# Kernel optimization log

Hardware: AMD Instinct MI355X
Metric: run time of the kernel (lower is better)

Reference implementation:

```python
import jax, jax.numpy as jnp
import numpy as np

N = 50000
E = 800000
DZ = 64
DH = 64


def setup_inputs() -> dict:
    key = jax.random.key(0)
    ks = jax.random.split(key, 10)
    z = jax.random.normal(ks[0], (N, DZ), dtype=jnp.float32)
    edge_src = jax.random.randint(ks[1], (E,), 0, N, dtype=jnp.int32)
    edge_dst = jax.random.randint(ks[2], (E,), 0, N, dtype=jnp.int32)
    # weights: normal(0, 0.1); biases: uniform(-0.1, 0.1) as in the torch init
    W_cur = 0.1 * jax.random.normal(ks[3], (DH, DZ), dtype=jnp.float32)
    b_cur = jax.random.uniform(ks[4], (DH,), minval=-0.1, maxval=0.1, dtype=jnp.float32)
    W_nbr = 0.1 * jax.random.normal(ks[5], (DH, 2 * DZ), dtype=jnp.float32)
    b_nbr = jax.random.uniform(ks[6], (DH,), minval=-0.1, maxval=0.1, dtype=jnp.float32)
    W_out = 0.1 * jax.random.normal(ks[7], (DZ, 2 * DH), dtype=jnp.float32)
    b_out = jax.random.uniform(ks[8], (DZ,), minval=-0.1, maxval=0.1, dtype=jnp.float32)
    return {"z": z, "edge_src": edge_src, "edge_dst": edge_dst,
            "W_cur": W_cur, "b_cur": b_cur, "W_nbr": W_nbr, "b_nbr": b_nbr,
            "W_out": W_out, "b_out": b_out}


def reference(z, edge_src, edge_dst, W_cur, b_cur, W_nbr, b_nbr, W_out, b_out):
    # self branch: Sigmoid(Linear(dim_z -> dim_h))  [N, DH]
    curvv = jax.nn.sigmoid(z @ W_cur.T + b_cur)
    # per-edge: concat(z[center], z[neighbor]) -> Sigmoid(Linear)  [E, DH]
    e = jnp.concatenate([z[edge_dst], z[edge_src]], axis=-1)  # [E, 2*DZ]
    m = jax.nn.sigmoid(e @ W_nbr.T + b_nbr)
    # sum-aggregate messages per center node (isolated nodes -> zeros)
    nbrvv = jax.ops.segment_sum(m, edge_dst, num_segments=N)  # [N, DH]
    # fuse: Tanh(Linear(concat(cur, nbr) -> dim_z))
    h = jnp.concatenate([curvv, nbrvv], axis=-1)  # [N, 2*DH]
    dzdt = jnp.tanh(h @ W_out.T + b_out)
    return dzdt
```

## Files before the change

kernel.cpp:

```cpp
#include <hip/hip_runtime.h>
#include <math.h>

#define NN 50000
#define NE 800000
#define BSH 7
#define NBUCK 391
#define CAP 4096
#define CHUNK 4096
#define NCH ((NE + CHUNK - 1) / CHUNK)
#define K1B 782
#define EPT2 8
#define SENT 50000

typedef float4 f4;
typedef float2 f2;
typedef unsigned short u16;
typedef unsigned int u32;

__device__ __forceinline__ float sigf(float x) {
    return __builtin_amdgcn_rcpf(1.0f + __expf(-x));
}

__device__ __forceinline__ u16 f32_to_bf16_rne(float f) {
    unsigned u = __float_as_uint(f);
    u += 0x7FFFu + ((u >> 16) & 1u);
    return (u16)(u >> 16);
}

#define K1_WFLOATS (3 * 32 * 64 * 2)
__global__ __launch_bounds__(512, 4) void k1_sc(
    const float* __restrict__ z,
    const float* __restrict__ Wc, const float* __restrict__ bc,
    const float* __restrict__ Wn, const float* __restrict__ bn,
    float* __restrict__ P, u16* __restrict__ Qh, float* __restrict__ C,
    const int* __restrict__ esrc, const int* __restrict__ edst,
    int* __restrict__ gcur, u32* __restrict__ ebuf)
{
    const int tid = threadIdx.x;
    if (blockIdx.x < K1B) {
        __shared__ float sh[K1_WFLOATS + 8 * 256];
        f2* w2 = (f2*)sh;
        for (int j = tid; j < 3 * 32 * 64; j += 512) {
            const int m = j >> 11, r = j & 2047;
            const int k2 = r >> 6, h = r & 63;
            const float* s = (m == 0) ? (Wc + h * 64 + 2 * k2)
                                      : (Wn + h * 128 + (m - 1) * 64 + 2 * k2);
            w2[(m * 32 + k2) * 64 + h] = *(const f2*)s;
        }
        __syncthreads();

        const int lane = tid & 63;
        const int wid  = tid >> 6;
        f4* tile = (f4*)(sh + K1_WFLOATS) + wid * 64;
        const f2* wl0 = w2;
        const f2* wl1 = w2 + 32 * 64;
        const f2* wl2 = w2 + 2 * 32 * 64;
        const float bcur = bc[lane], bnbr = bn[lane];

        const int gw = blockIdx.x * 8 + wid;
        const int nw = K1B * 8;
        for (int chunk = gw; chunk < NN / 4; chunk += nw) {
            const int n0 = chunk * 4;
            tile[lane] = *(const f4*)(z + n0 * 64 + lane * 4);
            float a0[4], a1[4], a2[4];
            #pragma unroll
            for (int ni = 0; ni < 4; ++ni) { a0[ni] = 0.f; a1[ni] = 0.f; a2[ni] = 0.f; }
            #pragma unroll 2
            for (int k4 = 0; k4 < 16; ++k4) {
                const f2 w0a = wl0[(2 * k4) * 64 + lane], w0b = wl0[(2 * k4 + 1) * 64 + lane];
                const f2 w1a = wl1[(2 * k4) * 64 + lane], w1b = wl1[(2 * k4 + 1) * 64 + lane];
                const f2 w2a = wl2[(2 * k4) * 64 + lane], w2b = wl2[(2 * k4 + 1) * 64 + lane];
                #pragma unroll
                for (int ni = 0; ni < 4; ++ni) {
                    const f4 zz = tile[ni * 16 + k4];
                    a0[ni] = fmaf(w0b.y, zz.w, fmaf(w0b.x, zz.z, fmaf(w0a.y, zz.y, fmaf(w0a.x, zz.x, a0[ni]))));
                    a1[ni] = fmaf(w1b.y, zz.w, fmaf(w1b.x, zz.z, fmaf(w1a.y, zz.y, fmaf(w1a.x, zz.x, a1[ni]))));
                    a2[ni] = fmaf(w2b.y, zz.w, fmaf(w2b.x, zz.z, fmaf(w2a.y, zz.y, fmaf(w2a.x, zz.x, a2[ni]))));
                }
            }
            #pragma unroll
            for (int ni = 0; ni < 4; ++ni) {
                const int n = n0 + ni;
                C[n * 64 + lane]  = sigf(a0[ni] + bcur);
                P[n * 64 + lane]  = a1[ni] + bnbr;
                Qh[n * 64 + lane] = f32_to_bf16_rne(a2[ni]);
            }
        }
    } else {
        if (blockIdx.x == K1B && tid < 64) Qh[(size_t)SENT * 64 + tid] = 0xFF80u;

        __shared__ int cnt[NBUCK];
        __shared__ int gbase[NBUCK];
        __shared__ int lcur[NBUCK];
        for (int i = tid; i < NBUCK; i += 512) cnt[i] = 0;
        __syncthreads();

        const int base = (blockIdx.x - K1B) * CHUNK;
        u32 ent[EPT2];
        int nb[EPT2];
        #pragma unroll
        for (int t = 0; t < EPT2; ++t) {
            const int e = base + t * 512 + tid;
            if (e < NE) {
                const int d = edst[e], s = esrc[e];
                const int b = d >> BSH;
                ent[t] = ((u32)(d & 127) << 16) | (u32)s;
                nb[t] = b;
                atomicAdd(&cnt[b], 1);
            } else {
                nb[t] = -1;
            }
        }
        __syncthreads();
        for (int i = tid; i < NBUCK; i += 512) {
            gbase[i] = cnt[i] ? atomicAdd(&gcur[i], cnt[i]) : 0;
            lcur[i] = 0;
        }
        __syncthreads();
        #pragma unroll
        for (int t = 0; t < EPT2; ++t) {
            if (nb[t] >= 0) {
                const int li = atomicAdd(&lcur[nb[t]], 1);
                ebuf[nb[t] * CAP + gbase[nb[t]] + li] = ent[t];
            }
        }
    }
}

__global__ __launch_bounds__(256) void k_bsort(const int* __restrict__ gcur,
                                               const u32* __restrict__ ebuf,
                                               u32* __restrict__ bd,
                                               u16* __restrict__ ss)
{
    __shared__ int hist[128];
    __shared__ int lcur[128];
    __shared__ int ps[128];
    __shared__ int tot;
    const int b = blockIdx.x;
    const int ecnt = gcur[b];
    const int e0 = b * CAP;
    const int n0 = b << BSH;
    const int t = threadIdx.x;

    if (t < 128) hist[t] = 0;
    __syncthreads();
    for (int j = t; j < ecnt; j += 256)
        atomicAdd(&hist[(ebuf[e0 + j] >> 16) & 127], 1);
    __syncthreads();
    if (t < 128) ps[t] = (hist[t] + 7) & ~7;
    __syncthreads();
    for (int o = 1; o < 128; o <<= 1) {
        int v = 0;
        if (t < 128 && t >= o) v = ps[t - o];
        __syncthreads();
        if (t < 128 && t >= o) ps[t] += v;
        __syncthreads();
    }
    if (t < 128) {
        const int a = hist[t];
        const int r = (a + 7) & ~7;
        const int excl = ps[t] - r;
        lcur[t] = excl;
        const int n = n0 + t;
        if (n < NN) bd[n] = ((u32)(e0 + excl) << 8) | (u32)a;
        if (t == 127) tot = ps[127];
    }
    __syncthreads();
    const int zw = (tot + 48) >> 1;
    u32* ssw = (u32*)(ss + e0);
    for (int j = t; j < zw; j += 256) ssw[j] = 0xC350C350u;
    __syncthreads();
    for (int j = t; j < ecnt; j += 256) {
        const u32 ent = ebuf[e0 + j];
        const int p = atomicAdd(&lcur[(ent >> 16) & 127], 1);
        ss[e0 + p] = (u16)(ent & 0xFFFFu);
    }
}

template<int NQ>
__device__ __forceinline__ void round_g(const u16* __restrict__ ip,
                                        const u16* __restrict__ qbl,
                                        float p, float& acc)
{
    uint4 iv0, iv1, iv2;
    asm volatile("global_load_dwordx4 %0, %1, off" : "=v"(iv0) : "v"(ip));
    if constexpr (NQ >= 16)
        asm volatile("global_load_dwordx4 %0, %1, off offset:16" : "=v"(iv1) : "v"(ip));
    if constexpr (NQ >= 24)
        asm volatile("global_load_dwordx4 %0, %1, off offset:32" : "=v"(iv2) : "v"(ip));
    asm volatile("s_waitcnt vmcnt(0)" ::: "memory");
    __builtin_amdgcn_sched_barrier(0);
    u32 wv[NQ / 2];
    wv[0] = iv0.x; wv[1] = iv0.y; wv[2] = iv0.z; wv[3] = iv0.w;
    if constexpr (NQ >= 16) { wv[4] = iv1.x; wv[5] = iv1.y; wv[6] = iv1.z; wv[7] = iv1.w; }
    if constexpr (NQ >= 24) { wv[8] = iv2.x; wv[9] = iv2.y; wv[10] = iv2.z; wv[11] = iv2.w; }
    u32 q[NQ];
    #pragma unroll
    for (int t8 = 0; t8 < NQ / 2; ++t8) {
        const u16* aL = qbl + ((wv[t8] & 0xFFFFu) << 6);
        const u16* aH = qbl + ((wv[t8] >> 16) << 6);
        asm volatile("global_load_ushort %0, %1, off" : "=v"(q[2 * t8])     : "v"(aL));
        asm volatile("global_load_ushort %0, %1, off" : "=v"(q[2 * t8 + 1]) : "v"(aH));
    }
    asm volatile("s_waitcnt vmcnt(0)" ::: "memory");
    __builtin_amdgcn_sched_barrier(0);
    #pragma unroll
    for (int t = 0; t < NQ; ++t)
        acc += sigf(p + __uint_as_float(q[t] << 16));
}

__global__ __launch_bounds__(512, 8) void k23(
    const u32* __restrict__ bd, const u16* __restrict__ ss,
    const float* __restrict__ P, const u16* __restrict__ Qh,
    const float* __restrict__ C, const float* __restrict__ Wo,
    const float* __restrict__ bo, float* __restrict__ out)
{
    __shared__ u32 w1u[32 * 64];
    __shared__ f2  w2f[32 * 64];
    __shared__ float tiles[8 * 512];
    const int tid = threadIdx.x;
    for (int j = tid; j < 32 * 64; j += 512) {
        const int k2 = j >> 6, d = j & 63;
        const f2 wc = *(const f2*)(Wo + d * 128 + 2 * k2);
        w1u[k2 * 64 + d] = ((u32)f32_to_bf16_rne(wc.y) << 16) | (u32)f32_to_bf16_rne(wc.x);
        w2f[k2 * 64 + d] = *(const f2*)(Wo + d * 128 + 64 + 2 * k2);
    }
    __syncthreads();

    const int lane = tid & 63;
    const int wid  = tid >> 6;
    float* tile = tiles + wid * 512;
    const f4* t4 = (const f4*)tile;
    const u16* qbl = Qh + lane;
    const float bout = bo[lane];

    for (int chunk = blockIdx.x * 8 + wid; chunk < NN / 4; chunk += gridDim.x * 8) {
        const int n0 = chunk * 4;
        #pragma unroll
        for (int i = 0; i < 4; ++i) {
            const int n = n0 + i;
            const u32 w = bd[n];
            const int beg = __builtin_amdgcn_readfirstlane((int)(w >> 8));
            const int dg  = __builtin_amdgcn_readfirstlane((int)(w & 255u));
            const int rdg = (dg + 7) & ~7;
            const float p = P[n * 64 + lane];
            tile[i * 128 + lane] = C[n * 64 + lane];
            float acc = 0.f;

            int jb = 0;
            for (; jb + 24 <= rdg; jb += 24)
                round_g<24>(ss + beg + jb, qbl, p, acc);
            const int rem = rdg - jb;
            if (rem == 16)     round_g<16>(ss + beg + jb, qbl, p, acc);
            else if (rem == 8) round_g<8>(ss + beg + jb, qbl, p, acc);

            tile[i * 128 + 64 + lane] = acc;
        }

        float a2[4] = {0.f, 0.f, 0.f, 0.f};
        #pragma unroll 2
        for (int k4 = 0; k4 < 16; ++k4) {
            const u32 ua = w1u[(2 * k4) * 64 + lane];
            const u32 ub = w1u[(2 * k4 + 1) * 64 + lane];
            const float wa0 = __uint_as_float(ua << 16);
            const float wa1 = __uint_as_float(ua & 0xFFFF0000u);
            const float wb0 = __uint_as_float(ub << 16);
            const float wb1 = __uint_as_float(ub & 0xFFFF0000u);
            #pragma unroll
            for (int i = 0; i < 4; ++i) {
                const f4 hv = t4[i * 32 + k4];
                a2[i] = fmaf(wb1, hv.w, fmaf(wb0, hv.z, fmaf(wa1, hv.y, fmaf(wa0, hv.x, a2[i]))));
            }
        }
        #pragma unroll 2
        for (int k4 = 0; k4 < 16; ++k4) {
            const f2 wa = w2f[(2 * k4) * 64 + lane];
            const f2 wb = w2f[(2 * k4 + 1) * 64 + lane];
            #pragma unroll
            for (int i = 0; i < 4; ++i) {
                const f4 hv = t4[i * 32 + 16 + k4];
                a2[i] = fmaf(wb.y, hv.w, fmaf(wb.x, hv.z, fmaf(wa.y, hv.y, fmaf(wa.x, hv.x, a2[i]))));
            }
        }
        #pragma unroll
        for (int i = 0; i < 4; ++i)
            out[(n0 + i) * 64 + lane] = tanhf(a2[i] + bout);
    }
}

extern "C" void kernel_launch(void* const* d_in, const int* in_sizes, int n_in,
                              void* d_out, int out_size, void* d_ws, size_t ws_size,
                              hipStream_t stream) {
    const float* z  = (const float*)d_in[0];
    const int* esrc = (const int*)d_in[1];
    const int* edst = (const int*)d_in[2];
    const float* Wc = (const float*)d_in[3];
    const float* bc = (const float*)d_in[4];
    const float* Wn = (const float*)d_in[5];
    const float* bn = (const float*)d_in[6];
    const float* Wo = (const float*)d_in[7];
    const float* bo = (const float*)d_in[8];
    float* out = (float*)d_out;

    float* P   = (float*)d_ws;
    float* C   = P + (size_t)NN * 64;
    u16* Qh    = (u16*)(C + (size_t)NN * 64);
    u32* bd    = (u32*)(Qh + (size_t)(NN + 1) * 64);
    int* gcur  = (int*)(bd + NN + 64);
    u32* ebuf  = (u32*)(gcur + 512);
    u16* ss    = (u16*)(ebuf + (size_t)NBUCK * CAP);

    hipMemsetAsync(gcur, 0, 512 * sizeof(int), stream);
    k1_sc<<<K1B + NCH, 512, 0, stream>>>(z, Wc, bc, Wn, bn, P, Qh, C,
                                         esrc, edst, gcur, ebuf);
    k_bsort<<<NBUCK, 256, 0, stream>>>(gcur, ebuf, bd, ss);
    k23<<<1563, 512, 0, stream>>>(bd, ss, P, Qh, C, Wo, bo, out);
}
```

Baseline: 106.6 us.

## Prefetch next node's edge indices and prescale logits for raw exp2 sigmoid

Every node's padded edge list now takes at least 24 slots, so the gather kernel can issue one fixed 24-wide round per node and prefetch the next node's index block while the current Q gathers are in flight. Outlier nodes with more than 24 edges fall back to the old loop. P and Q are pre-multiplied by -log2(e) so the sigmoid can use v_exp_f32 directly, dropping a multiply per edge, and the sentinel changes to +inf so padded slots still contribute zero. The cost is more padding, so more sentinel gathers and more wasted sigmoids for low-degree nodes (average degree is about 16), plus a larger padded index buffer.

Result: slower. 109.3 us (+2.6%).

```diff
diff --git a/kernel.cpp b/kernel.cpp
--- a/kernel.cpp
+++ b/kernel.cpp
@@ -11,6 +11,7 @@
 #define K1B 782
 #define EPT2 8
 #define SENT 50000
+#define NL2E -1.4426950408889634f
 
 typedef float4 f4;
 typedef float2 f2;
@@ -19,6 +20,12 @@
 
 __device__ __forceinline__ float sigf(float x) {
     return __builtin_amdgcn_rcpf(1.0f + __expf(-x));
+}
+
+__device__ __forceinline__ float sigf2(float y) {
+    float e;
+    asm("v_exp_f32 %0, %1" : "=v"(e) : "v"(y));
+    return __builtin_amdgcn_rcpf(1.0f + e);
 }
 
 __device__ __forceinline__ u16 f32_to_bf16_rne(float f) {
@@ -82,12 +89,12 @@
             for (int ni = 0; ni < 4; ++ni) {
                 const int n = n0 + ni;
                 C[n * 64 + lane]  = sigf(a0[ni] + bcur);
-                P[n * 64 + lane]  = a1[ni] + bnbr;
-                Qh[n * 64 + lane] = f32_to_bf16_rne(a2[ni]);
+                P[n * 64 + lane]  = (a1[ni] + bnbr) * NL2E;
+                Qh[n * 64 + lane] = f32_to_bf16_rne(a2[ni] * NL2E);
             }
         }
     } else {
-        if (blockIdx.x == K1B && tid < 64) Qh[(size_t)SENT * 64 + tid] = 0xFF80u;
+        if (blockIdx.x == K1B && tid < 64) Qh[(size_t)SENT * 64 + tid] = 0x7F80u;
 
         __shared__ int cnt[NBUCK];
         __shared__ int gbase[NBUCK];
@@ -147,7 +154,10 @@
     for (int j = t; j < ecnt; j += 256)
         atomicAdd(&hist[(ebuf[e0 + j] >> 16) & 127], 1);
     __syncthreads();
-    if (t < 128) ps[t] = (hist[t] + 7) & ~7;
+    if (t < 128) {
+        const int a = hist[t];
+        ps[t] = (a <= 24) ? 24 : ((a + 7) & ~7);
+    }
     __syncthreads();
     for (int o = 1; o < 128; o <<= 1) {
         int v = 0;
@@ -158,7 +168,7 @@
     }
     if (t < 128) {
         const int a = hist[t];
-        const int r = (a + 7) & ~7;
+        const int r = (a <= 24) ? 24 : ((a + 7) & ~7);
         const int excl = ps[t] - r;
         lcur[t] = excl;
         const int n = n0 + t;
@@ -206,7 +216,7 @@
     __builtin_amdgcn_sched_barrier(0);
     #pragma unroll
     for (int t = 0; t < NQ; ++t)
-        acc += sigf(p + __uint_as_float(q[t] << 16));
+        acc += sigf2(p + __uint_as_float(q[t] << 16));
 }
 
 __global__ __launch_bounds__(512, 8) void k23(
@@ -236,24 +246,61 @@
 
     for (int chunk = blockIdx.x * 8 + wid; chunk < NN / 4; chunk += gridDim.x * 8) {
         const int n0 = chunk * 4;
+        int beg[4], dg[4];
+        float pv[4];
         #pragma unroll
         for (int i = 0; i < 4; ++i) {
-            const int n = n0 + i;
-            const u32 w = bd[n];
-            const int beg = __builtin_amdgcn_readfirstlane((int)(w >> 8));
-            const int dg  = __builtin_amdgcn_readfirstlane((int)(w & 255u));
-            const int rdg = (dg + 7) & ~7;
-            const float p = P[n * 64 + lane];
-            tile[i * 128 + lane] = C[n * 64 + lane];
+            const u32 w = bd[n0 + i];
+            beg[i] = __builtin_amdgcn_readfirstlane((int)(w >> 8));
+            dg[i]  = __builtin_amdgcn_readfirstlane((int)(w & 255u));
+            pv[i]  = P[(n0 + i) * 64 + lane];
+            tile[i * 128 + lane] = C[(n0 + i) * 64 + lane];
+        }
+
+        uint4 iv0, iv1, iv2;
+        {
+            const u16* ip = ss + beg[0];
+            asm volatile("global_load_dwordx4 %0, %1, off" : "=v"(iv0) : "v"(ip));
+            asm volatile("global_load_dwordx4 %0, %1, off offset:16" : "=v"(iv1) : "v"(ip));
+            asm volatile("global_load_dwordx4 %0, %1, off offset:32" : "=v"(iv2) : "v"(ip));
+        }
+        #pragma unroll
+        for (int i = 0; i < 4; ++i) {
+            asm volatile("s_waitcnt vmcnt(0)" ::: "memory");
+            __builtin_amdgcn_sched_barrier(0);
+            u32 q[24];
+            #define G2(w, k) { \
+                const u16* aL = qbl + (((w) & 0xFFFFu) << 6); \
+                const u16* aH = qbl + (((w) >> 16) << 6); \
+                asm volatile("global_load_ushort %0, %1, off" : "=v"(q[k])     : "v"(aL)); \
+                asm volatile("global_load_ushort %0, %1, off" : "=v"(q[(k)+1]) : "v"(aH)); }
+            G2(iv0.x, 0)  G2(iv0.y, 2)  G2(iv0.z, 4)  G2(iv0.w, 6)
+            G2(iv1.x, 8)  G2(iv1.y, 10) G2(iv1.z, 12) G2(iv1.w, 14)
+            G2(iv2.x, 16) G2(iv2.y, 18) G2(iv2.z, 20) G2(iv2.w, 22)
+            #undef G2
+            if (i < 3) {
+                const u16* ip = ss + beg[i + 1];
+                asm volatile("global_load_dwordx4 %0, %1, off" : "=v"(iv0) : "v"(ip));
+                asm volatile("global_load_dwordx4 %0, %1, off offset:16" : "=v"(iv1) : "v"(ip));
+                asm volatile("global_load_dwordx4 %0, %1, off offset:32" : "=v"(iv2) : "v"(ip));
+                asm volatile("s_waitcnt vmcnt(3)" ::: "memory");
+            } else {
+                asm volatile("s_waitcnt vmcnt(0)" ::: "memory");
+            }
+            __builtin_amdgcn_sched_barrier(0);
             float acc = 0.f;
-
-            int jb = 0;
-            for (; jb + 24 <= rdg; jb += 24)
-                round_g<24>(ss + beg + jb, qbl, p, acc);
-            const int rem = rdg - jb;
-            if (rem == 16)     round_g<16>(ss + beg + jb, qbl, p, acc);
-            else if (rem == 8) round_g<8>(ss + beg + jb, qbl, p, acc);
-
+            #pragma unroll
+            for (int t = 0; t < 24; ++t)
+                acc += sigf2(pv[i] + __uint_as_float(q[t] << 16));
+            if (dg[i] > 24) {
+                const int rdg = (dg[i] + 7) & ~7;
+                int jb = 24;
+                for (; jb + 24 <= rdg; jb += 24)
+                    round_g<24>(ss + beg[i] + jb, qbl, pv[i], acc);
+                const int rem = rdg - jb;
+                if (rem == 16)     round_g<16>(ss + beg[i] + jb, qbl, pv[i], acc);
+                else if (rem == 8) round_g<8>(ss + beg[i] + jb, qbl, pv[i], acc);
+            }
             tile[i * 128 + 64 + lane] = acc;
         }
 
```

## Gather two bf16 channels per dword and prescale logits by -log2e

Applied to the files above, without the earlier changes.

The edge-gather loop now has each lane fetch a dword (two bf16 channels) for one edge, with the two half-waves taking alternate edges. Partial sums are combined with a cross-half shuffle. This halves the number of gather instructions per edge row. P and Q are also stored prescaled by -log2(e), so the sigmoid uses a raw v_exp_f32 without a multiply, and the padding sentinel becomes +inf so padded edges still contribute zero. In exchange it adds a shuffle and selection logic per node, and changes the bf16 rounding point of Q slightly.

Result: faster. 102.7 us (-3.7%).

```diff
diff --git a/kernel.cpp b/kernel.cpp
--- a/kernel.cpp
+++ b/kernel.cpp
@@ -11,6 +11,7 @@
 #define K1B 782
 #define EPT2 8
 #define SENT 50000
+#define NL2E -1.4426950408889634f
 
 typedef float4 f4;
 typedef float2 f2;
@@ -19,6 +20,12 @@
 
 __device__ __forceinline__ float sigf(float x) {
     return __builtin_amdgcn_rcpf(1.0f + __expf(-x));
+}
+
+__device__ __forceinline__ float sigf2(float y) {
+    float e;
+    asm("v_exp_f32 %0, %1" : "=v"(e) : "v"(y));
+    return __builtin_amdgcn_rcpf(1.0f + e);
 }
 
 __device__ __forceinline__ u16 f32_to_bf16_rne(float f) {
@@ -82,12 +89,12 @@
             for (int ni = 0; ni < 4; ++ni) {
                 const int n = n0 + ni;
                 C[n * 64 + lane]  = sigf(a0[ni] + bcur);
-                P[n * 64 + lane]  = a1[ni] + bnbr;
-                Qh[n * 64 + lane] = f32_to_bf16_rne(a2[ni]);
+                P[n * 64 + lane]  = (a1[ni] + bnbr) * NL2E;
+                Qh[n * 64 + lane] = f32_to_bf16_rne(a2[ni] * NL2E);
             }
         }
     } else {
-        if (blockIdx.x == K1B && tid < 64) Qh[(size_t)SENT * 64 + tid] = 0xFF80u;
+        if (blockIdx.x == K1B && tid < 64) Qh[(size_t)SENT * 64 + tid] = 0x7F80u;
 
         __shared__ int cnt[NBUCK];
         __shared__ int gbase[NBUCK];
@@ -177,36 +184,40 @@
     }
 }
 
-template<int NQ>
-__device__ __forceinline__ void round_g(const u16* __restrict__ ip,
-                                        const u16* __restrict__ qbl,
-                                        float p, float& acc)
+template<int NW>
+__device__ __forceinline__ void round_g2(const u16* __restrict__ ip,
+                                         const u16* __restrict__ qbl2,
+                                         int sel, f2 p2,
+                                         float& acc0, float& acc1)
 {
     uint4 iv0, iv1, iv2;
     asm volatile("global_load_dwordx4 %0, %1, off" : "=v"(iv0) : "v"(ip));
-    if constexpr (NQ >= 16)
+    if constexpr (NW >= 8)
         asm volatile("global_load_dwordx4 %0, %1, off offset:16" : "=v"(iv1) : "v"(ip));
-    if constexpr (NQ >= 24)
+    if constexpr (NW >= 12)
         asm volatile("global_load_dwordx4 %0, %1, off offset:32" : "=v"(iv2) : "v"(ip));
     asm volatile("s_waitcnt vmcnt(0)" ::: "memory");
     __builtin_amdgcn_sched_barrier(0);
-    u32 wv[NQ / 2];
+    u32 wv[NW];
     wv[0] = iv0.x; wv[1] = iv0.y; wv[2] = iv0.z; wv[3] = iv0.w;
-    if constexpr (NQ >= 16) { wv[4] = iv1.x; wv[5] = iv1.y; wv[6] = iv1.z; wv[7] = iv1.w; }
-    if constexpr (NQ >= 24) { wv[8] = iv2.x; wv[9] = iv2.y; wv[10] = iv2.z; wv[11] = iv2.w; }
-    u32 q[NQ];
+    if constexpr (NW >= 8)  { wv[4] = iv1.x; wv[5] = iv1.y; wv[6] = iv1.z; wv[7] = iv1.w; }
+    if constexpr (NW >= 12) { wv[8] = iv2.x; wv[9] = iv2.y; wv[10] = iv2.z; wv[11] = iv2.w; }
+    u32 q[NW];
     #pragma unroll
-    for (int t8 = 0; t8 < NQ / 2; ++t8) {
-        const u16* aL = qbl + ((wv[t8] & 0xFFFFu) << 6);
-        const u16* aH = qbl + ((wv[t8] >> 16) << 6);
-        asm volatile("global_load_ushort %0, %1, off" : "=v"(q[2 * t8])     : "v"(aL));
-        asm volatile("global_load_ushort %0, %1, off" : "=v"(q[2 * t8 + 1]) : "v"(aH));
+    for (int w = 0; w < NW; ++w) {
+        const u32 sv = (wv[w] >> sel) & 0xFFFFu;
+        const u16* a = qbl2 + (sv << 6);
+        asm volatile("global_load_dword %0, %1, off" : "=v"(q[w]) : "v"(a));
     }
     asm volatile("s_waitcnt vmcnt(0)" ::: "memory");
     __builtin_amdgcn_sched_barrier(0);
     #pragma unroll
-    for (int t = 0; t < NQ; ++t)
-        acc += sigf(p + __uint_as_float(q[t] << 16));
+    for (int w = 0; w < NW; ++w) {
+        const float lo = __uint_as_float(q[w] << 16);
+        const float hi = __uint_as_float(q[w] & 0xFFFF0000u);
+        acc0 += sigf2(p2.x + lo);
+        acc1 += sigf2(p2.y + hi);
+    }
 }
 
 __global__ __launch_bounds__(512, 8) void k23(
@@ -231,7 +242,8 @@
     const int wid  = tid >> 6;
     float* tile = tiles + wid * 512;
     const f4* t4 = (const f4*)tile;
-    const u16* qbl = Qh + lane;
+    const int sel = (lane >= 32) ? 16 : 0;
+    const u16* qbl2 = Qh + (lane & 31) * 2;
     const float bout = bo[lane];
 
     for (int chunk = blockIdx.x * 8 + wid; chunk < NN / 4; chunk += gridDim.x * 8) {
@@ -243,18 +255,23 @@
             const int beg = __builtin_amdgcn_readfirstlane((int)(w >> 8));
             const int dg  = __builtin_amdgcn_readfirstlane((int)(w & 255u));
             const int rdg = (dg + 7) & ~7;
-            const float p = P[n * 64 + lane];
+            const f2 p2 = *(const f2*)(P + n * 64 + 2 * (lane & 31));
             tile[i * 128 + lane] = C[n * 64 + lane];
-            float acc = 0.f;
+            float acc0 = 0.f, acc1 = 0.f;
 
             int jb = 0;
             for (; jb + 24 <= rdg; jb += 24)
-                round_g<24>(ss + beg + jb, qbl, p, acc);
+                round_g2<12>(ss + beg + jb, qbl2, sel, p2, acc0, acc1);
             const int rem = rdg - jb;
-            if (rem == 16)     round_g<16>(ss + beg + jb, qbl, p, acc);
-            else if (rem == 8) round_g<8>(ss + beg + jb, qbl, p, acc);
-
-            tile[i * 128 + 64 + lane] = acc;
+            if (rem == 16)     round_g2<8>(ss + beg + jb, qbl2, sel, p2, acc0, acc1);
+            else if (rem == 8) round_g2<4>(ss + beg + jb, qbl2, sel, p2, acc0, acc1);
+
+            const float s0 = __shfl_xor(acc0, 32, 64);
+            const float s1 = __shfl_xor(acc1, 32, 64);
+            if (lane < 32) {
+                f2 v; v.x = acc0 + s0; v.y = acc1 + s1;
+                *(f2*)(tile + i * 128 + 64 + 2 * lane) = v;
+            }
         }
 
         float a2[4] = {0.f, 0.f, 0.f, 0.f};
```
